# Optimization experiments

Hardware: AMD Instinct MI355X
Metric: run time of the kernel (lower is better)

## Reference

```python
import jax, jax.numpy as jnp
import numpy as np
from jax import lax

DIST_THRESH = 180.0
ATT_THRESH = 0.05


def setup_inputs() -> dict:
    key = jax.random.key(0)
    ks = jax.random.split(key, 6)
    B, N, H, W = 16, 512, 25, 25
    F, Fh = H * W, int(H * W * 1.5)  # 625, 937
    x4 = jax.random.normal(ks[0], (B, N, H, W), dtype=jnp.float32) * 0.25
    attention = jax.random.uniform(ks[1], (B, N, 1, 1), dtype=jnp.float32)
    W1 = jax.random.normal(ks[2], (2, F, Fh), dtype=jnp.float32) * (1.0 / np.sqrt(F))
    b1 = jnp.zeros((Fh,), dtype=jnp.float32)
    W2 = jax.random.normal(ks[3], (2, Fh, F), dtype=jnp.float32) * (1.0 / np.sqrt(Fh))
    b2 = jnp.zeros((F,), dtype=jnp.float32)
    return {"x4": x4, "attention": attention, "W1": W1, "b1": b1, "W2": W2, "b2": b2}


def _build_adjacency(X, att):
    """X: [B,N,F] node features, att: [B,N]. Returns thresholded adjacency [B,N,N]."""
    B, N, F = X.shape
    # pairwise L1 distances, row-by-row scan to avoid materializing [B,N,N,F]
    Xs = jnp.swapaxes(X, 0, 1)  # [N,B,F]

    def row(_, xi):  # xi: [B,F]
        d = jnp.sum(jnp.abs(xi[:, None, :] - X), axis=-1)  # [B,N]
        return None, d

    _, D = lax.scan(row, None, Xs)          # [N,B,N]
    D = jnp.swapaxes(D, 0, 1)               # [B,N,N]
    att_d = jnp.abs(att[:, :, None] - att[:, None, :])  # [B,N,N]
    A = ((D <= DIST_THRESH) & (att_d <= ATT_THRESH)).astype(jnp.float32)
    # original only fills i<j and j<i, diagonal stays 0
    A = A * (1.0 - jnp.eye(N, dtype=jnp.float32))
    return A


def _process_graph(A):
    """A + I, then row-normalize by inverse degree (D^-1 (A+I))."""
    N = A.shape[1]
    A = A + jnp.eye(N, dtype=A.dtype)
    deg = jnp.sum(A, axis=-1)               # [B,N]
    dinv = jnp.where(deg > 0, 1.0 / deg, 0.0)
    return dinv[:, :, None] * A


def _cheb_conv(x, L, Wk, b):
    """ChebConv with K=2 over dense normalized graph L: T0=x, T1=Lx."""
    t1 = jnp.einsum('bij,bjf->bif', L, x)
    return jnp.einsum('bnf,fo->bno', x, Wk[0]) + jnp.einsum('bnf,fo->bno', t1, Wk[1]) + b


def reference(x4, attention, W1, b1, W2, b2):
    B, N, H, W = x4.shape
    X = x4.reshape(B, N, H * W)             # [B,N,625] flow_x
    att = attention[:, :, 0, 0]             # [B,N]
    A = _build_adjacency(X, att)
    L = _process_graph(A)
    h = jax.nn.relu(_cheb_conv(X, L, W1, b1))   # [B,N,937]
    out = jax.nn.relu(_cheb_conv(h, L, W2, b2))  # [B,N,625]
    return out
```

## Files before the change

kernel.cpp:

```cpp
#include <hip/hip_runtime.h>
#include <stdint.h>

typedef uint16_t u16;
typedef uint32_t u32;
typedef __attribute__((ext_vector_type(4))) float f32x4;
typedef __attribute__((ext_vector_type(4))) unsigned short us4;
typedef __attribute__((ext_vector_type(8))) unsigned short us8;

#define NB   16
#define NN   512
#define FF   625
#define FH   937
#define ROWS 8192
#define KS1  1280
#define KS2  1920
#define NPX  640
#define NPH  960
#define F4   160
#define GQ   4

using frag_ab = __attribute__((ext_vector_type(8))) short;
using frag_cd = __attribute__((ext_vector_type(4))) float;

__device__ __forceinline__ u16 f32_bf16(float f) {
  union { float f; uint32_t u; } x; x.f = f;
  uint32_t r = x.u + 0x7fffu + ((x.u >> 16) & 1u);
  return (u16)(r >> 16);
}
__device__ __forceinline__ void gload_lds16(const void* g, void* l) {
  __builtin_amdgcn_global_load_lds((__attribute__((address_space(1))) void*)g,
                                   (__attribute__((address_space(3))) void*)l,
                                   16, 0, 0);
}

__global__ __launch_bounds__(256) void prep(
    const float* __restrict__ x4, const float* __restrict__ att,
    const float* __restrict__ W1, const float* __restrict__ W2,
    f32x4* __restrict__ Xpad, u16* __restrict__ Xcat, u16* __restrict__ Xt,
    u16* __restrict__ W1t, u16* __restrict__ W2t,
    u16* __restrict__ order, float* __restrict__ att_s)
{
  __shared__ __align__(16) float smem[2112];
  const int blk = blockIdx.x;
  const int tid = threadIdx.x;

  if (blk < 16) {
    float* a_sh = smem;
    const int b = blk;
    a_sh[tid]       = att[b * NN + tid];
    a_sh[tid + 256] = att[b * NN + tid + 256];
    __syncthreads();
    #pragma unroll
    for (int h = 0; h < 2; ++h) {
      const int i = tid + h * 256;
      const float ai = a_sh[i];
      int r = 0;
      for (int j = 0; j < NN; ++j) {
        const float aj = a_sh[j];
        r += (aj < ai) || (aj == ai && j < i);
      }
      order[(size_t)b * NN + r] = (u16)i;
      att_s[(size_t)b * NN + r] = ai;
    }
  } else if (blk < 1040) {
    float* T = smem;
    const int idx = blk - 16;
    const int xcd = idx & 7, sub = idx >> 3;
    const int b = xcd * 2 + (sub >> 6);
    const int rr = sub & 63;
    const int q = rr >> 4;
    const int nt = rr & 15;
    const int node0 = nt * 32;
    const int tx = tid & 31, ty = tid >> 5;
    const int lrow = tid >> 3, lcol = tid & 7;

    int buf = 0;
    {
      const int f0 = q * 160;
      #pragma unroll
      for (int r = 0; r < 4; ++r) {
        const int node = node0 + ty + r * 8;
        const int f = f0 + tx;
        T[(ty + r * 8) * 33 + tx] = (f < FF) ? x4[((size_t)b * NN + node) * FF + f] : 0.f;
      }
    }
    __syncthreads();

    for (int c = 0; c < 5; ++c) {
      const int f0 = q * 160 + c * 32;
      float vnext[4];
      const bool has = (c + 1 < 5);
      if (has) {
        const int fn = f0 + 32 + tx;
        #pragma unroll
        for (int r = 0; r < 4; ++r) {
          const int node = node0 + ty + r * 8;
          vnext[r] = (fn < FF) ? x4[((size_t)b * NN + node) * FF + fn] : 0.f;
        }
      }
      {
        const int node_l = lrow, k4s = lcol;
        const size_t grow = (size_t)b * NN + node0 + node_l;
        const int k4 = q * 40 + c * 8 + k4s;
        f32x4 v; us4 o;
        #pragma unroll
        for (int t = 0; t < 4; ++t) {
          const float x = T[buf * 1056 + node_l * 33 + k4s * 4 + t];
          v[t] = x; o[t] = f32_bf16(x);
        }
        Xpad[grow * F4 + k4] = v;
        *(us4*)(Xcat + grow * KS1 + k4 * 4) = o;
      }
      {
        const int fl = lrow, nl = lcol;
        const int f = f0 + fl;
        us4 ov;
        #pragma unroll
        for (int t = 0; t < 4; ++t)
          ov[t] = f32_bf16(T[buf * 1056 + (nl * 4 + t) * 33 + fl]);
        *(us4*)(Xt + ((size_t)b * NPX + f) * 512 + node0 + nl * 4) = ov;
      }
      if (has) {
        #pragma unroll
        for (int r = 0; r < 4; ++r)
          T[(buf ^ 1) * 1056 + (ty + r * 8) * 33 + tx] = vnext[r];
        __syncthreads();
        buf ^= 1;
      }
    }
  } else if (blk < 2320) {
    float (*tile)[33] = (float(*)[33])smem;
    const int bb = blk - 1040;
    const int kt = bb % 40, nt = bb / 40;
    const int tx = tid & 31, ty = tid >> 5;
    #pragma unroll
    for (int r = 0; r < 4; ++r) {
      int k = kt * 32 + ty + r * 8;
      int n = nt * 32 + tx;
      float v = 0.f;
      int c = -1, kk = 0;
      if (k < 625) { c = 0; kk = k; }
      else if (k >= 640 && k < 1265) { c = 1; kk = k - 640; }
      if (c >= 0 && n < FH) v = W1[((size_t)c * 625 + kk) * FH + n];
      tile[ty + r * 8][tx] = v;
    }
    __syncthreads();
    #pragma unroll
    for (int r = 0; r < 4; ++r) {
      int n = nt * 32 + ty + r * 8;
      int k = kt * 32 + tx;
      W1t[(size_t)n * KS1 + k] = f32_bf16(tile[tx][ty + r * 8]);
    }
  } else {
    float (*tile)[33] = (float(*)[33])smem;
    const int bb = blk - 2320;
    const int kt = bb % 60, nt = bb / 60;
    const int tx = tid & 31, ty = tid >> 5;
    #pragma unroll
    for (int r = 0; r < 4; ++r) {
      int k = kt * 32 + ty + r * 8;
      int n = nt * 32 + tx;
      float v = 0.f;
      int c = -1, kk = 0;
      if (k < 937) { c = 0; kk = k; }
      else if (k >= 960 && k < 1897) { c = 1; kk = k - 960; }
      if (c >= 0 && n < FF) v = W2[((size_t)c * 937 + kk) * FF + n];
      tile[ty + r * 8][tx] = v;
    }
    __syncthreads();
    #pragma unroll
    for (int r = 0; r < 4; ++r) {
      int n = nt * 32 + ty + r * 8;
      int k = kt * 32 + tx;
      W2t[(size_t)n * KS2 + k] = f32_bf16(tile[tx][ty + r * 8]);
    }
  }
}

__global__ __launch_bounds__(256) void build_L(
    const f32x4* __restrict__ Xpad,
    const u16* __restrict__ order,
    const float* __restrict__ att_s,
    u16* __restrict__ L)
{
  __shared__ float atts[512];
  __shared__ u16 ords[512];
  __shared__ u16 cand[512];
  __shared__ u16 flag[GQ][512];
  __shared__ int ncand, naccs[GQ];

  const int tid = threadIdx.x;
  const int blk = blockIdx.x;
  const int xcd = blk & 7, sub = blk >> 3;
  const int b = xcd * 2 + (sub >> 7);
  const int p0 = (sub & 127) * GQ;
  const f32x4* Xb4 = Xpad + (size_t)b * NN * F4;

  atts[tid]       = att_s[b * NN + tid];
  atts[tid + 256] = att_s[b * NN + tid + 256];
  ords[tid]       = order[b * NN + tid];
  ords[tid + 256] = order[b * NN + tid + 256];
  {
    u32* fz = (u32*)&flag[0][0];
    #pragma unroll
    for (int s = 0; s < GQ; ++s) fz[tid + s * 256] = 0;
  }
  if (tid == 0) ncand = 0;
  if (tid < GQ) naccs[tid] = 0;
  __syncthreads();

  float av[GQ]; int ig[GQ];
  #pragma unroll
  for (int g = 0; g < GQ; ++g) { av[g] = atts[p0 + g]; ig[g] = ords[p0 + g]; }
  if (tid < GQ) flag[tid][ords[p0 + tid]] = 1;

  {
    const float lo = av[0] - 0.0501f, hi = av[GQ - 1] + 0.0501f;
    const bool q0 = (atts[tid] >= lo) && (atts[tid] <= hi);
    const bool q1 = (atts[tid + 256] >= lo) && (atts[tid + 256] <= hi);
    const unsigned long long m0 = __ballot(q0);
    const unsigned long long m1 = __ballot(q1);
    const int c0 = __popcll(m0);
    const int c1 = __popcll(m1);
    const int lane = tid & 63;
    int base = 0;
    if (lane == 0 && (c0 + c1)) base = atomicAdd(&ncand, c0 + c1);
    base = __shfl(base, 0, 64);
    const unsigned long long below = (1ull << lane) - 1ull;
    if (q0) cand[base + __popcll(m0 & below)] = (u16)tid;
    if (q1) cand[base + c0 + __popcll(m1 & below)] = (u16)(tid + 256);
  }
  __syncthreads();
  const int nc = ncand;

  const int hl = tid & 31;
  const int hw = tid >> 5;

  f32x4 xi[GQ][5];
  #pragma unroll
  for (int g = 0; g < GQ; ++g) {
    const f32x4* Xi = Xb4 + (size_t)ig[g] * F4;
    #pragma unroll
    for (int s = 0; s < 5; ++s) xi[g][s] = Xi[s * 32 + hl];
  }

  for (int c = hw; c < nc; c += 8) {
    const int p = cand[c];
    const int j = ords[p];
    const float aj = atts[p];
    const f32x4* Xj = Xb4 + (size_t)j * F4;
    f32x4 xj[5];
    #pragma unroll
    for (int s = 0; s < 5; ++s) xj[s] = Xj[s * 32 + hl];

    float pd[GQ];
    #pragma unroll
    for (int g = 0; g < GQ; ++g) {
      float p2 = 0.f;
      #pragma unroll
      for (int t = 0; t < 4; ++t) {
        p2 += fabsf(xi[g][0][t] - xj[0][t]) + fabsf(xi[g][1][t] - xj[1][t])
            + fabsf(xi[g][2][t] - xj[2][t]) + fabsf(xi[g][3][t] - xj[3][t])
            + fabsf(xi[g][4][t] - xj[4][t]);
      }
      pd[g] = p2;
    }
    #pragma unroll
    for (int off = 16; off; off >>= 1) {
      #pragma unroll
      for (int g = 0; g < GQ; ++g) pd[g] += __shfl_xor(pd[g], off, 64);
    }
    if (hl == 0) {
      #pragma unroll
      for (int g = 0; g < GQ; ++g) {
        if (pd[g] <= 180.0f && fabsf(av[g] - aj) <= 0.05f && j != ig[g]) {
          flag[g][j] = 1;
          atomicAdd(&naccs[g], 1);
        }
      }
    }
  }
  __syncthreads();

  #pragma unroll
  for (int g = 0; g < GQ; ++g) {
    const u16 dv = f32_bf16(1.0f / (float)(naccs[g] + 1));
    const long row = (long)b * NN + ig[g];
    const u32 lo2 = flag[g][2 * tid]     ? (u32)dv : 0u;
    const u32 hi2 = flag[g][2 * tid + 1] ? (u32)dv : 0u;
    *(u32*)(L + (size_t)row * 512 + 2 * tid) = lo2 | (hi2 << 16);
  }
}

template <int KS, int NTILE, int NREAL, int NSTORE, bool RELU, bool BIAS,
          bool OUT_BF16, bool WT>
__device__ __forceinline__ void gemm_core(
    const u16* __restrict__ At,
    const u16* __restrict__ Btt,
    const float* __restrict__ bias, void* __restrict__ C,
    u16* __restrict__ Ct,
    long crow0, int col0, int ldc)
{
  constexpr int NI = NTILE / 32;
  constexpr int BR = NTILE / 32;
  __shared__ __align__(16) u16 Ash[128 * 64];
  __shared__ __align__(16) u16 Bsh[NTILE * 64];

  const int tid  = threadIdx.x;
  const int lane = tid & 63;
  const int wave = tid >> 6;
  const int wm = wave & 1, wn = wave >> 1;
  const int q = lane >> 4, l16 = lane & 15;

  const u16* pa[4]; const u16* pb[BR];
  #pragma unroll
  for (int r = 0; r < 4; ++r) {
    const int ci = r * 256 + tid;
    const int row = ci >> 3, cpos = ci & 7;
    pa[r] = At + (size_t)row * KS + (cpos ^ (row & 7)) * 8;
  }
  #pragma unroll
  for (int r = 0; r < BR; ++r) {
    const int ci = r * 256 + tid;
    const int row = ci >> 3, cpos = ci & 7;
    pb[r] = Btt + (size_t)row * KS + (cpos ^ (row & 7)) * 8;
  }
  const int wbase = (tid & 192) * 8;

  const frag_ab* fA[4][2]; const frag_ab* fB[NI][2];
  #pragma unroll
  for (int mi = 0; mi < 4; ++mi) {
    const int row = wm * 64 + mi * 16 + l16;
    fA[mi][0] = (const frag_ab*)&Ash[row * 64 + ((q    ) ^ (l16 & 7)) * 8];
    fA[mi][1] = (const frag_ab*)&Ash[row * 64 + ((q + 4) ^ (l16 & 7)) * 8];
  }
  #pragma unroll
  for (int ni = 0; ni < NI; ++ni) {
    const int row = wn * (NTILE / 2) + ni * 16 + l16;
    fB[ni][0] = (const frag_ab*)&Bsh[row * 64 + ((q    ) ^ (l16 & 7)) * 8];
    fB[ni][1] = (const frag_ab*)&Bsh[row * 64 + ((q + 4) ^ (l16 & 7)) * 8];
  }

  frag_cd acc[4][NI] = {};

  constexpr int KT = KS / 64;
  for (int kt = 0; kt < KT; ++kt) {
    __syncthreads();
    #pragma unroll
    for (int r = 0; r < 4; ++r) { gload_lds16(pa[r], &Ash[r * 2048 + wbase]); pa[r] += 64; }
    #pragma unroll
    for (int r = 0; r < BR; ++r) { gload_lds16(pb[r], &Bsh[r * 2048 + wbase]); pb[r] += 64; }
    __syncthreads();

    #pragma unroll
    for (int kk = 0; kk < 2; ++kk) {
      frag_ab av[4], bv[NI];
      #pragma unroll
      for (int mi = 0; mi < 4; ++mi) av[mi] = *fA[mi][kk];
      #pragma unroll
      for (int ni = 0; ni < NI; ++ni) bv[ni] = *fB[ni][kk];
      #pragma unroll
      for (int mi = 0; mi < 4; ++mi)
        #pragma unroll
        for (int ni = 0; ni < NI; ++ni)
          acc[mi][ni] = __builtin_amdgcn_mfma_f32_16x16x32_bf16(
              av[mi], bv[ni], acc[mi][ni], 0, 0, 0);
    }
  }

  #pragma unroll
  for (int ni = 0; ni < NI; ++ni) {
    const int col = col0 + wn * (NTILE / 2) + ni * 16 + l16;
    if (col >= NSTORE) continue;
    const bool ok = (col < NREAL);
    float bvv = 0.f;
    if (BIAS) bvv = ok ? bias[col] : 0.f;
    #pragma unroll
    for (int mi = 0; mi < 4; ++mi) {
      us4 tv;
      #pragma unroll
      for (int r = 0; r < 4; ++r) {
        const long rowg = crow0 + wm * 64 + mi * 16 + q * 4 + r;
        float v = acc[mi][ni][r];
        if (BIAS) v += bvv;
        if (RELU) v = fmaxf(v, 0.f);
        if (!ok) v = 0.f;
        if (OUT_BF16) {
          const u16 v16 = f32_bf16(v);
          ((u16*)C)[rowg * (size_t)ldc + col] = v16;
          if (WT) tv[r] = v16;
        } else {
          ((float*)C)[rowg * (size_t)ldc + col] = v;
        }
      }
      if (WT) {
        const long bb = crow0 >> 9;
        const int node = (int)(crow0 & 511) + wm * 64 + mi * 16 + q * 4;
        *(us4*)(Ct + ((size_t)bb * NPH + col) * 512 + node) = tv;
      }
    }
  }
}

template <int KS, int NTILE, int NREAL, int NSTORE, bool RELU, bool BIAS,
          bool OUT_BF16, bool WT>
__global__ __launch_bounds__(256) void gemm_dense(
    const u16* __restrict__ A, const u16* __restrict__ Bt,
    const float* __restrict__ bias, void* __restrict__ C,
    u16* __restrict__ Ct, int ldc)
{
  const int x = blockIdx.x;
  const int mt = ((x & 7) << 3) | (x >> 3);
  gemm_core<KS, NTILE, NREAL, NSTORE, RELU, BIAS, OUT_BF16, WT>(
      A + (size_t)mt * 128 * KS, Bt + (size_t)blockIdx.y * NTILE * KS,
      bias, C, Ct, (long)mt * 128, blockIdx.y * NTILE, ldc);
}

template <int NP>
__global__ __launch_bounds__(256) void spmm(
    const u16* __restrict__ L, const u16* __restrict__ Bt,
    u16* __restrict__ C, int ldc)
{
  constexpr int TPB = 4 * (NP / 64);
  const int blk = blockIdx.x;
  const int xcd = blk & 7, sub = blk >> 3;
  const int b = xcd * 2 + sub / TPB;
  const int t = sub % TPB;
  const int mt = t & 3, nt = t >> 2;
  gemm_core<512, 64, NP, NP, false, false, true, false>(
      L + ((size_t)b * 512 + mt * 128) * 512,
      Bt + ((size_t)b * NP + nt * 64) * 512,
      nullptr, C, nullptr, (long)b * 512 + mt * 128, nt * 64, ldc);
}

extern "C" void kernel_launch(void* const* d_in, const int* in_sizes, int n_in,
                              void* d_out, int out_size, void* d_ws, size_t ws_size,
                              hipStream_t stream) {
  const float* x4  = (const float*)d_in[0];
  const float* att = (const float*)d_in[1];
  const float* W1  = (const float*)d_in[2];
  const float* b1  = (const float*)d_in[3];
  const float* W2  = (const float*)d_in[4];
  const float* b2  = (const float*)d_in[5];
  float* out = (float*)d_out;

  char* ws = (char*)d_ws;
  f32x4* Xpad = (f32x4*)ws;
  u16* ht = (u16*)ws;       ws += (size_t)ROWS * F4 * 16;
  u16* Xcat = (u16*)ws;  ws += (size_t)ROWS * KS1 * 2;
  u16* hcat = (u16*)ws;  ws += (size_t)ROWS * KS2 * 2;
  u16* W1t  = (u16*)ws;  ws += (size_t)1024 * KS1 * 2;
  u16* W2t  = (u16*)ws;  ws += (size_t)640 * KS2 * 2;
  u16* Lm   = (u16*)ws;  ws += (size_t)NB * 512 * 512 * 2;
  u16* Xt   = (u16*)ws;  ws += (size_t)NB * NPX * 512 * 2;
  float* att_s = (float*)ws; ws += (size_t)NB * NN * 4;
  u16* order_  = (u16*)ws;   ws += (size_t)NB * NN * 2;

  prep<<<dim3(3520), 256, 0, stream>>>(x4, att, W1, W2, Xpad, Xcat, Xt,
                                       W1t, W2t, order_, att_s);
  build_L<<<dim3(2048), 256, 0, stream>>>(Xpad, order_, att_s, Lm);
  spmm<NPX><<<dim3(640), 256, 0, stream>>>(Lm, Xt, Xcat + NPX, KS1);
  gemm_dense<KS1, 128, FH, NPH, true, true, true, true><<<dim3(64, 8), 256, 0, stream>>>(
      Xcat, W1t, b1, (void*)hcat, ht, KS2);
  spmm<NPH><<<dim3(960), 256, 0, stream>>>(Lm, ht, hcat + NPH, KS2);
  gemm_dense<KS2, 64, FF, FF, true, true, false, false><<<dim3(64, 10), 256, 0, stream>>>(
      hcat, W2t, b2, (void*)out, nullptr, FF);
}
```

Measured before the change: 218.4 us.

## Double-buffer LDS tiles in GEMM core to overlap global loads with MFMA

Splits the A and B shared-memory tiles into two buffers. The next K-slice is issued into the alternate buffer before the MFMAs run on the current one, and only one barrier is kept per iteration. This is meant to hide global-to-LDS load latency behind matrix compute. It doubles LDS use per block, which may lower occupancy. It also relies on the async LDS loads having completed by the time of the single barrier.

```diff
diff --git a/kernel.cpp b/kernel.cpp
--- a/kernel.cpp
+++ b/kernel.cpp
@@ -303,8 +303,8 @@
 {
   constexpr int NI = NTILE / 32;
   constexpr int BR = NTILE / 32;
-  __shared__ __align__(16) u16 Ash[128 * 64];
-  __shared__ __align__(16) u16 Bsh[NTILE * 64];
+  __shared__ __align__(16) u16 Ash[2][128 * 64];
+  __shared__ __align__(16) u16 Bsh[2][NTILE * 64];
 
   const int tid  = threadIdx.x;
   const int lane = tid & 63;
@@ -327,38 +327,47 @@
   }
   const int wbase = (tid & 192) * 8;
 
-  const frag_ab* fA[4][2]; const frag_ab* fB[NI][2];
+  int aoff[4][2], boff[NI][2];
   #pragma unroll
   for (int mi = 0; mi < 4; ++mi) {
     const int row = wm * 64 + mi * 16 + l16;
-    fA[mi][0] = (const frag_ab*)&Ash[row * 64 + ((q    ) ^ (l16 & 7)) * 8];
-    fA[mi][1] = (const frag_ab*)&Ash[row * 64 + ((q + 4) ^ (l16 & 7)) * 8];
+    aoff[mi][0] = row * 64 + ((q    ) ^ (l16 & 7)) * 8;
+    aoff[mi][1] = row * 64 + ((q + 4) ^ (l16 & 7)) * 8;
   }
   #pragma unroll
   for (int ni = 0; ni < NI; ++ni) {
     const int row = wn * (NTILE / 2) + ni * 16 + l16;
-    fB[ni][0] = (const frag_ab*)&Bsh[row * 64 + ((q    ) ^ (l16 & 7)) * 8];
-    fB[ni][1] = (const frag_ab*)&Bsh[row * 64 + ((q + 4) ^ (l16 & 7)) * 8];
+    boff[ni][0] = row * 64 + ((q    ) ^ (l16 & 7)) * 8;
+    boff[ni][1] = row * 64 + ((q + 4) ^ (l16 & 7)) * 8;
   }
 
   frag_cd acc[4][NI] = {};
-
   constexpr int KT = KS / 64;
+
+  #pragma unroll
+  for (int r = 0; r < 4; ++r) { gload_lds16(pa[r], &Ash[0][r * 2048 + wbase]); pa[r] += 64; }
+  #pragma unroll
+  for (int r = 0; r < BR; ++r) { gload_lds16(pb[r], &Bsh[0][r * 2048 + wbase]); pb[r] += 64; }
+  __syncthreads();
+
+  int cur = 0;
   for (int kt = 0; kt < KT; ++kt) {
-    __syncthreads();
-    #pragma unroll
-    for (int r = 0; r < 4; ++r) { gload_lds16(pa[r], &Ash[r * 2048 + wbase]); pa[r] += 64; }
-    #pragma unroll
-    for (int r = 0; r < BR; ++r) { gload_lds16(pb[r], &Bsh[r * 2048 + wbase]); pb[r] += 64; }
-    __syncthreads();
-
+    if (kt + 1 < KT) {
+      const int nxt = cur ^ 1;
+      #pragma unroll
+      for (int r = 0; r < 4; ++r) { gload_lds16(pa[r], &Ash[nxt][r * 2048 + wbase]); pa[r] += 64; }
+      #pragma unroll
+      for (int r = 0; r < BR; ++r) { gload_lds16(pb[r], &Bsh[nxt][r * 2048 + wbase]); pb[r] += 64; }
+    }
+    const u16* A0 = &Ash[cur][0];
+    const u16* B0 = &Bsh[cur][0];
     #pragma unroll
     for (int kk = 0; kk < 2; ++kk) {
       frag_ab av[4], bv[NI];
       #pragma unroll
-      for (int mi = 0; mi < 4; ++mi) av[mi] = *fA[mi][kk];
-      #pragma unroll
-      for (int ni = 0; ni < NI; ++ni) bv[ni] = *fB[ni][kk];
+      for (int mi = 0; mi < 4; ++mi) av[mi] = *(const frag_ab*)&A0[aoff[mi][kk]];
+      #pragma unroll
+      for (int ni = 0; ni < NI; ++ni) bv[ni] = *(const frag_ab*)&B0[boff[ni][kk]];
       #pragma unroll
       for (int mi = 0; mi < 4; ++mi)
         #pragma unroll
@@ -366,6 +375,8 @@
           acc[mi][ni] = __builtin_amdgcn_mfma_f32_16x16x32_bf16(
               av[mi], bv[ni], acc[mi][ni], 0, 0, 0);
     }
+    __syncthreads();
+    cur ^= 1;
   }
 
   #pragma unroll
```

After: 239.9 us. 1.1x slower.

## Fuse first-layer graph aggregation into build_L and drop transposed X copy

Applied to the files above, without the earlier changes.

Computes L·X for the first ChebConv inside build_L by summing the fp32 feature rows of the accepted candidate neighbors, scaling by inverse degree, and writing bf16 directly into the second half of Xcat. This removes the first spmm launch and the prep stage that produced the transposed bf16 Xt buffer. The prep kernel is simplified to a plain row-wise conversion with more blocks. In exchange, build_L does extra gather work per row, iterating over all candidates with per-group flag checks, and accumulates in fp32 from the fp32 copy rather than using the MFMA spmm.

```diff
diff --git a/kernel.cpp b/kernel.cpp
--- a/kernel.cpp
+++ b/kernel.cpp
@@ -5,7 +5,6 @@
 typedef uint32_t u32;
 typedef __attribute__((ext_vector_type(4))) float f32x4;
 typedef __attribute__((ext_vector_type(4))) unsigned short us4;
-typedef __attribute__((ext_vector_type(8))) unsigned short us8;
 
 #define NB   16
 #define NN   512
@@ -36,11 +35,11 @@
 __global__ __launch_bounds__(256) void prep(
     const float* __restrict__ x4, const float* __restrict__ att,
     const float* __restrict__ W1, const float* __restrict__ W2,
-    f32x4* __restrict__ Xpad, u16* __restrict__ Xcat, u16* __restrict__ Xt,
+    f32x4* __restrict__ Xpad, u16* __restrict__ Xcat,
     u16* __restrict__ W1t, u16* __restrict__ W2t,
     u16* __restrict__ order, float* __restrict__ att_s)
 {
-  __shared__ __align__(16) float smem[2112];
+  __shared__ __align__(16) float smem[1056];
   const int blk = blockIdx.x;
   const int tid = threadIdx.x;
 
@@ -62,75 +61,26 @@
       order[(size_t)b * NN + r] = (u16)i;
       att_s[(size_t)b * NN + r] = ai;
     }
-  } else if (blk < 1040) {
-    float* T = smem;
+  } else if (blk < 4112) {
     const int idx = blk - 16;
-    const int xcd = idx & 7, sub = idx >> 3;
-    const int b = xcd * 2 + (sub >> 6);
-    const int rr = sub & 63;
-    const int q = rr >> 4;
-    const int nt = rr & 15;
-    const int node0 = nt * 32;
-    const int tx = tid & 31, ty = tid >> 5;
-    const int lrow = tid >> 3, lcol = tid & 7;
-
-    int buf = 0;
-    {
-      const int f0 = q * 160;
-      #pragma unroll
-      for (int r = 0; r < 4; ++r) {
-        const int node = node0 + ty + r * 8;
-        const int f = f0 + tx;
-        T[(ty + r * 8) * 33 + tx] = (f < FF) ? x4[((size_t)b * NN + node) * FF + f] : 0.f;
-      }
-    }
-    __syncthreads();
-
-    for (int c = 0; c < 5; ++c) {
-      const int f0 = q * 160 + c * 32;
-      float vnext[4];
-      const bool has = (c + 1 < 5);
-      if (has) {
-        const int fn = f0 + 32 + tx;
-        #pragma unroll
-        for (int r = 0; r < 4; ++r) {
-          const int node = node0 + ty + r * 8;
-          vnext[r] = (fn < FF) ? x4[((size_t)b * NN + node) * FF + fn] : 0.f;
-        }
-      }
-      {
-        const int node_l = lrow, k4s = lcol;
-        const size_t grow = (size_t)b * NN + node0 + node_l;
-        const int k4 = q * 40 + c * 8 + k4s;
-        f32x4 v; us4 o;
-        #pragma unroll
-        for (int t = 0; t < 4; ++t) {
-          const float x = T[buf * 1056 + node_l * 33 + k4s * 4 + t];
-          v[t] = x; o[t] = f32_bf16(x);
-        }
-        Xpad[grow * F4 + k4] = v;
-        *(us4*)(Xcat + grow * KS1 + k4 * 4) = o;
-      }
-      {
-        const int fl = lrow, nl = lcol;
-        const int f = f0 + fl;
-        us4 ov;
-        #pragma unroll
-        for (int t = 0; t < 4; ++t)
-          ov[t] = f32_bf16(T[buf * 1056 + (nl * 4 + t) * 33 + fl]);
-        *(us4*)(Xt + ((size_t)b * NPX + f) * 512 + node0 + nl * 4) = ov;
-      }
-      if (has) {
-        #pragma unroll
-        for (int r = 0; r < 4; ++r)
-          T[(buf ^ 1) * 1056 + (ty + r * 8) * 33 + tx] = vnext[r];
-        __syncthreads();
-        buf ^= 1;
-      }
-    }
-  } else if (blk < 2320) {
+    const int xcd = idx & 7, loc = idx >> 3;
+    const int row0 = xcd * 1024 + loc * 2;
+    for (int s = tid; s < 320; s += 256) {
+      const int row = row0 + (s >= 160);
+      const int k4 = (s >= 160) ? s - 160 : s;
+      f32x4 v; us4 o;
+      #pragma unroll
+      for (int t = 0; t < 4; ++t) {
+        const int f = k4 * 4 + t;
+        float x = (f < FF) ? x4[(size_t)row * FF + f] : 0.f;
+        v[t] = x; o[t] = f32_bf16(x);
+      }
+      Xpad[(size_t)row * F4 + k4] = v;
+      *(us4*)(Xcat + (size_t)row * KS1 + k4 * 4) = o;
+    }
+  } else if (blk < 5392) {
     float (*tile)[33] = (float(*)[33])smem;
-    const int bb = blk - 1040;
+    const int bb = blk - 4112;
     const int kt = bb % 40, nt = bb / 40;
     const int tx = tid & 31, ty = tid >> 5;
     #pragma unroll
@@ -153,7 +103,7 @@
     }
   } else {
     float (*tile)[33] = (float(*)[33])smem;
-    const int bb = blk - 2320;
+    const int bb = blk - 5392;
     const int kt = bb % 60, nt = bb / 60;
     const int tx = tid & 31, ty = tid >> 5;
     #pragma unroll
@@ -181,7 +131,8 @@
     const f32x4* __restrict__ Xpad,
     const u16* __restrict__ order,
     const float* __restrict__ att_s,
-    u16* __restrict__ L)
+    u16* __restrict__ L,
+    u16* __restrict__ Xcat)
 {
   __shared__ float atts[512];
   __shared__ u16 ords[512];
@@ -290,6 +241,29 @@
     const u32 hi2 = flag[g][2 * tid + 1] ? (u32)dv : 0u;
     *(u32*)(L + (size_t)row * 512 + 2 * tid) = lo2 | (hi2 << 16);
   }
+
+  {
+    const float* Xbf = (const float*)Xb4;
+    float a0[GQ] = {}, a1[GQ] = {}, a2[GQ] = {};
+    for (int c = 0; c < nc; ++c) {
+      const int j = ords[cand[c]];
+      const float v0 = Xbf[(size_t)j * 640 + tid];
+      const float v1 = Xbf[(size_t)j * 640 + tid + 256];
+      const float v2 = (tid < 128) ? Xbf[(size_t)j * 640 + tid + 512] : 0.f;
+      #pragma unroll
+      for (int g = 0; g < GQ; ++g) {
+        if (flag[g][j]) { a0[g] += v0; a1[g] += v1; a2[g] += v2; }
+      }
+    }
+    #pragma unroll
+    for (int g = 0; g < GQ; ++g) {
+      const float dv = 1.0f / (float)(naccs[g] + 1);
+      u16* dst = Xcat + ((size_t)b * NN + ig[g]) * KS1 + 640;
+      dst[tid]       = f32_bf16(dv * a0[g]);
+      dst[tid + 256] = f32_bf16(dv * a1[g]);
+      if (tid < 128) dst[tid + 512] = f32_bf16(dv * a2[g]);
+    }
+  }
 }
 
 template <int KS, int NTILE, int NREAL, int NSTORE, bool RELU, bool BIAS,
@@ -452,14 +426,12 @@
   u16* W1t  = (u16*)ws;  ws += (size_t)1024 * KS1 * 2;
   u16* W2t  = (u16*)ws;  ws += (size_t)640 * KS2 * 2;
   u16* Lm   = (u16*)ws;  ws += (size_t)NB * 512 * 512 * 2;
-  u16* Xt   = (u16*)ws;  ws += (size_t)NB * NPX * 512 * 2;
   float* att_s = (float*)ws; ws += (size_t)NB * NN * 4;
   u16* order_  = (u16*)ws;   ws += (size_t)NB * NN * 2;
 
-  prep<<<dim3(3520), 256, 0, stream>>>(x4, att, W1, W2, Xpad, Xcat, Xt,
+  prep<<<dim3(6592), 256, 0, stream>>>(x4, att, W1, W2, Xpad, Xcat,
                                        W1t, W2t, order_, att_s);
-  build_L<<<dim3(2048), 256, 0, stream>>>(Xpad, order_, att_s, Lm);
-  spmm<NPX><<<dim3(640), 256, 0, stream>>>(Lm, Xt, Xcat + NPX, KS1);
+  build_L<<<dim3(2048), 256, 0, stream>>>(Xpad, order_, att_s, Lm, Xcat);
   gemm_dense<KS1, 128, FH, NPH, true, true, true, true><<<dim3(64, 8), 256, 0, stream>>>(
       Xcat, W1t, b1, (void*)hcat, ht, KS2);
   spmm<NPH><<<dim3(960), 256, 0, stream>>>(Lm, ht, hcat + NPH, KS2);
```

New measurement: 237.2 us. +8.6%, slower.
